# Kernel tuning notes

Hardware: AMD Instinct MI355X
Metric: run time of the kernel (lower is better)

The kernel has to match this reference:

```python
import jax, jax.numpy as jnp
import numpy as np

EPS = 1e-5
R_MAX = 2.0
KPTS = 4

def silu(x):
    return x * jax.nn.sigmoid(x)

def conv1x1(x, w):  # w: (O, I)
    return jnp.einsum('oi,bihw->bohw', w, x)

def dwconv3(x, k):  # k: (C, 1, 3, 3), depthwise
    return jax.lax.conv_general_dilated(x, k, (1, 1), 'SAME',
        feature_group_count=x.shape[1], dimension_numbers=('NCHW', 'OIHW', 'NCHW'))

def conv3x3(x, k):  # k: (O, I, 3, 3)
    return jax.lax.conv_general_dilated(x, k, (1, 1), 'SAME',
        dimension_numbers=('NCHW', 'OIHW', 'NCHW'))

def bn_eval(x, g, b, m, v):
    scale = g / jnp.sqrt(v + EPS)
    return x * scale[None, :, None, None] + (b - m * scale)[None, :, None, None]

def ds_block(x, dw, pw, g, b, m, v):  # _DS: dwconv3 -> 1x1 -> BN -> SiLU
    return silu(bn_eval(conv1x1(dwconv3(x, dw), pw), g, b, m, v))

def offset_attn_head(q, w1, w2, b2):
    h = silu(conv3x3(q, w1))
    out = conv1x1(h, w2) + b2[None, :, None, None]
    B, _, H, W = out.shape
    off = out[:, :2 * KPTS].reshape(B, KPTS, 2, H, W)
    w = jax.nn.softmax(out[:, 2 * KPTS:].reshape(B, KPTS, H, W), axis=1)
    return off, w

def make_base_grid(Hf, Wf, Hc, Wc):
    yy, xx = jnp.meshgrid(jnp.arange(Hf, dtype=jnp.float32),
                          jnp.arange(Wf, dtype=jnp.float32), indexing='ij')
    xc = (xx + 0.5) * (Wc / Wf) - 0.5
    yc = (yy + 0.5) * (Hc / Hf) - 0.5
    gx = 2.0 * xc / max(Wc - 1, 1) - 1.0
    gy = 2.0 * yc / max(Hc - 1, 1) - 1.0
    return jnp.stack((gx, gy), axis=-1)  # (Hf, Wf, 2)

def avgpool(x, f):  # exact adaptive_avg_pool2d when H,W divisible by f
    B, C, H, W = x.shape
    return x.reshape(B, C, H // f, f, W // f, f).mean(axis=(3, 5))

def _gather(imgf, idx):  # imgf (C, HW), idx (K, Hf, Wf) -> (C, K, Hf, Wf)
    return imgf[:, idx]

def deform_sample(coarse, off, w, base, r_max=R_MAX):
    # bilinear grid_sample, padding_mode='border', align_corners=True
    B, C, Hc, Wc = coarse.shape
    K = off.shape[1]
    step_x = 2.0 / max(Wc - 1, 1)
    step_y = 2.0 / max(Hc - 1, 1)
    gx = base[..., 0][None, None] + jnp.tanh(off[:, :, 0]) * (r_max * step_x)  # (B,K,Hf,Wf)
    gy = base[..., 1][None, None] + jnp.tanh(off[:, :, 1]) * (r_max * step_y)
    ix = jnp.clip((gx + 1.0) * 0.5 * (Wc - 1), 0.0, Wc - 1)  # border padding = clamp
    iy = jnp.clip((gy + 1.0) * 0.5 * (Hc - 1), 0.0, Hc - 1)
    x0 = jnp.floor(ix); y0 = jnp.floor(iy)
    wx = (ix - x0)[:, None]  # (B,1,K,Hf,Wf)
    wy = (iy - y0)[:, None]
    x0i = x0.astype(jnp.int32); y0i = y0.astype(jnp.int32)
    x1i = jnp.minimum(x0i + 1, Wc - 1); y1i = jnp.minimum(y0i + 1, Hc - 1)
    imgf = coarse.reshape(B, C, Hc * Wc)
    g = jax.vmap(_gather)
    v00 = g(imgf, y0i * Wc + x0i)  # (B,C,K,Hf,Wf)
    v01 = g(imgf, y0i * Wc + x1i)
    v10 = g(imgf, y1i * Wc + x0i)
    v11 = g(imgf, y1i * Wc + x1i)
    samp = (v00 * (1 - wx) * (1 - wy) + v01 * wx * (1 - wy)
            + v10 * (1 - wx) * wy + v11 * wx * wy)
    return jnp.einsum('bkhw,bckhw->bchw', w, samp)

def csdm(x, ds0_dw, ds0_pw, ds0_g, ds0_b, ds0_m, ds0_v,
         ds1_dw, ds1_pw, ds1_g, ds1_b, ds1_m, ds1_v,
         ds2_dw, ds2_pw, ds2_g, ds2_b, ds2_m, ds2_v,
         qproj_w, h1_w1, h1_w2, h1_b2, h2_w1, h2_w2, h2_b2,
         r_w1, r_b1, r_w2, r_b2, final_w):
    B, C, H, W = x.shape
    s1 = avgpool(x, 2)
    s2 = avgpool(x, 4)
    z0 = ds_block(x,  ds0_dw, ds0_pw, ds0_g, ds0_b, ds0_m, ds0_v)
    z1 = ds_block(s1, ds1_dw, ds1_pw, ds1_g, ds1_b, ds1_m, ds1_v)
    z2 = ds_block(s2, ds2_dw, ds2_pw, ds2_g, ds2_b, ds2_m, ds2_v)
    q = conv1x1(z0, qproj_w)
    off1, w1 = offset_attn_head(q, h1_w1, h1_w2, h1_b2)
    off2, w2 = offset_attn_head(q, h2_w1, h2_w2, h2_b2)
    base1 = make_base_grid(H, W, z1.shape[2], z1.shape[3])
    base2 = make_base_grid(H, W, z2.shape[2], z2.shape[3])
    y1 = deform_sample(z1, off1, w1, base1)
    y2 = deform_sample(z2, off2, w2, base2)
    d0 = z0.mean(axis=(2, 3))
    d1 = y1.mean(axis=(2, 3))
    d2 = y2.mean(axis=(2, 3))
    hid = silu(jnp.concatenate([d0, d1, d2], axis=-1) @ r_w1 + r_b1)
    alpha = jax.nn.softmax(hid @ r_w2 + r_b2, axis=-1)  # (B, 3)
    a = alpha[:, :, None, None, None]
    out = a[:, 0] * z0 + a[:, 1] * y1 + a[:, 2] * y2
    return x + conv1x1(out, final_w)

def setup_inputs() -> dict:
    key = jax.random.key(0)
    B, C, H, W = 4, 32, 256, 256
    h, hr = 16, 32  # head hidden = max(4, int(C*0.5)); router hidden = max(16, C)
    ks = jax.random.split(key, 40)
    n = lambda i, shape, s=0.2: jax.random.normal(ks[i], shape, jnp.float32) * s
    inp = {'x': jax.random.normal(ks[0], (B, C, H, W), jnp.float32)}
    for j, p in enumerate(['ds0', 'ds1', 'ds2']):
        b = 1 + 6 * j
        inp[p + '_dw'] = n(b, (C, 1, 3, 3))
        inp[p + '_pw'] = n(b + 1, (C, C))
        inp[p + '_g'] = jnp.ones((C,), jnp.float32)
        inp[p + '_b'] = jnp.zeros((C,), jnp.float32)
        inp[p + '_m'] = n(b + 4, (C,), 0.1)
        inp[p + '_v'] = 1.0 + jax.random.uniform(ks[b + 5], (C,), jnp.float32) * 0.1
    inp['qproj_w'] = n(20, (C, C))
    inp['h1_w1'] = n(21, (h, C, 3, 3)); inp['h1_w2'] = n(22, (3 * KPTS, h)); inp['h1_b2'] = n(23, (3 * KPTS,), 0.1)
    inp['h2_w1'] = n(24, (h, C, 3, 3)); inp['h2_w2'] = n(25, (3 * KPTS, h)); inp['h2_b2'] = n(26, (3 * KPTS,), 0.1)
    inp['r_w1'] = n(27, (3 * C, hr)); inp['r_b1'] = n(28, (hr,), 0.1)
    inp['r_w2'] = n(29, (hr, 3)); inp['r_b2'] = n(30, (3,), 0.1)
    inp['final_w'] = n(31, (C, C))
    return inp

def reference(x, ds0_dw, ds0_pw, ds0_g, ds0_b, ds0_m, ds0_v,
              ds1_dw, ds1_pw, ds1_g, ds1_b, ds1_m, ds1_v,
              ds2_dw, ds2_pw, ds2_g, ds2_b, ds2_m, ds2_v,
              qproj_w, h1_w1, h1_w2, h1_b2, h2_w1, h2_w2, h2_b2,
              r_w1, r_b1, r_w2, r_b2, final_w):
    return csdm(x, ds0_dw, ds0_pw, ds0_g, ds0_b, ds0_m, ds0_v,
                ds1_dw, ds1_pw, ds1_g, ds1_b, ds1_m, ds1_v,
                ds2_dw, ds2_pw, ds2_g, ds2_b, ds2_m, ds2_v,
                qproj_w, h1_w1, h1_w2, h1_b2, h2_w1, h2_w2, h2_b2,
                r_w1, r_b1, r_w2, r_b2, final_w)
```

## Files before the change

kernel.cpp:

```cpp
#include <hip/hip_runtime.h>
#include <math.h>


constexpr int B = 4, C = 32, H = 256, W = 256;
constexpr int HW = H * W;
constexpr int H1 = 128, W1 = 128, HW1 = H1 * W1;
constexpr int H2 = 64,  W2 = 64,  HW2 = H2 * W2;
constexpr int CH = 16;
constexpr int CO = 12;
constexpr int TILE = 16;
constexpr int HALO = 18;
constexpr int TAREA = HALO * HALO;
constexpr int WP = 258;

typedef unsigned short ushort_t;
typedef __attribute__((ext_vector_type(8))) short bf16x8;
typedef __attribute__((ext_vector_type(4))) float f32x4;
typedef __attribute__((ext_vector_type(2))) float v2f;

static __device__ __forceinline__ float fast_rcp(float x) { return __builtin_amdgcn_rcpf(x); }
static __device__ __forceinline__ float silu_f(float x) { return x * fast_rcp(1.0f + __expf(-x)); }
static __device__ __forceinline__ v2f silu2(v2f x) {
    v2f r; r.x = silu_f(x.x); r.y = silu_f(x.y); return r;
}
static __device__ __forceinline__ float tanh_f(float x) {
    float xc = fminf(fmaxf(x, -15.0f), 15.0f);
    float e = __expf(2.0f * xc);
    return (e - 1.0f) * fast_rcp(e + 1.0f);
}
static __device__ __forceinline__ ushort_t f2b(float f) {
    unsigned u = __float_as_uint(f);
    return (ushort_t)((u + 0x7fffu + ((u >> 16) & 1u)) >> 16);
}
static __device__ __forceinline__ float bl(unsigned u) { return __uint_as_float(u << 16); }
static __device__ __forceinline__ float bh(unsigned u) { return __uint_as_float(u & 0xffff0000u); }

static __device__ __forceinline__ float red8_ch(float v0, float v1, float v2, float v3,
                                                float v4, float v5, float v6, float v7,
                                                int lane) {
    bool q0 = (lane & 1) != 0, q1 = (lane & 2) != 0, q2 = (lane & 4) != 0;
    float a0 = (q0 ? v4 : v0) + __shfl_xor(q0 ? v0 : v4, 1, 64);
    float a1 = (q0 ? v5 : v1) + __shfl_xor(q0 ? v1 : v5, 1, 64);
    float a2 = (q0 ? v6 : v2) + __shfl_xor(q0 ? v2 : v6, 1, 64);
    float a3 = (q0 ? v7 : v3) + __shfl_xor(q0 ? v3 : v7, 1, 64);
    float c0 = (q1 ? a2 : a0) + __shfl_xor(q1 ? a0 : a2, 2, 64);
    float c1 = (q1 ? a3 : a1) + __shfl_xor(q1 ? a1 : a3, 2, 64);
    float e  = (q2 ? c1 : c0) + __shfl_xor(q2 ? c0 : c1, 4, 64);
    e += __shfl_xor(e, 8, 64);
    e += __shfl_xor(e, 16, 64);
    e += __shfl_xor(e, 32, 64);
    return e;
}

__global__ void pre_kernel(const float* __restrict__ x, float* __restrict__ s1,
                           float* __restrict__ s2,
                           ushort_t* __restrict__ qpad, float* __restrict__ dall,
                           const float* __restrict__ h1w1, const float* __restrict__ h2w1,
                           ushort_t* __restrict__ w1ra, ushort_t* __restrict__ w1rb) {
    int idx = blockIdx.x * blockDim.x + threadIdx.x;
    constexpr int NP = B * C * HW1;
    constexpr int NP2 = B * C * HW2;
    if (idx < NP) {
        int wo = idx % W1; int t = idx / W1;
        int ho = t % H1;   t /= H1;
        const float* src = x + ((size_t)t * H + (size_t)ho * 2) * W + (size_t)wo * 2;
        s1[idx] = (src[0] + src[1] + src[W] + src[W + 1]) * 0.25f;
        return;
    }
    int i = idx - NP;
    if (i < NP2) {
        int wo = i % W2; int t = i / W2;
        int ho = t % H2;   t /= H2;
        const float* src = x + ((size_t)t * H + (size_t)ho * 4) * W + (size_t)wo * 4;
        float s = 0.0f;
#pragma unroll
        for (int r = 0; r < 4; ++r) {
            const float* rp = src + (size_t)r * W;
            s += (rp[0] + rp[1]) + (rp[2] + rp[3]);
        }
        s2[i] = s * 0.0625f;
        return;
    }
    i -= NP2;
    if (i < 4112) {
        int b = i / 1028, r = i % 1028;
        int y, xx;
        if (r < 258)      { y = 0;           xx = r; }
        else if (r < 516) { y = 257;         xx = r - 258; }
        else if (r < 772) { y = r - 516 + 1; xx = 0; }
        else              { y = r - 772 + 1; xx = 257; }
        uint4 z4 = {0, 0, 0, 0};
        uint4* p = (uint4*)(qpad + (((size_t)b * WP + y) * WP + xx) * 32);
        p[0] = z4; p[1] = z4; p[2] = z4; p[3] = z4;
        return;
    }
    i -= 4112;
    if (i < 512) { dall[i] = 0.0f; return; }
    i -= 512;
    if (i < 4608) {
        int o = i / 288, k = i - o * 288;
        int j = k >> 5, ci = k & 31;
        w1ra[i] = f2b(h1w1[(o * C + ci) * 9 + j]);
        return;
    }
    i -= 4608;
    if (i < 4608) {
        int o = i / 288, k = i - o * 288;
        int j = k >> 5, ci = k & 31;
        w1rb[i] = f2b(h2w1[(o * C + ci) * 9 + j]);
    }
}

struct DsParams {
    const float* in; const float* dw; const float* pw;
    const float* g;  const float* b;  const float* m; const float* v;
};

__global__ __launch_bounds__(256, 4) void fused_ds_all_kernel(
        DsParams P0, DsParams P1, DsParams P2, const float* __restrict__ qw,
        float* __restrict__ z0out, ushort_t* __restrict__ z1cl,
        ushort_t* __restrict__ z2cl, ushort_t* __restrict__ qout,
        float* __restrict__ dall) {
    __shared__ unsigned tileu[16 * TAREA];
    __shared__ v2f dwp[16 * 9];
    __shared__ v2f pwp[C * 16];
    __shared__ v2f qwp[C * 16];
    __shared__ v2f scale2[16], shift2[16];
    __shared__ float zsum[4][32];

    int bx = blockIdx.x;
    int level = (bx < 1024) ? 0 : (bx < 1280 ? 1 : 2);
    int rel = bx - ((level == 0) ? 0 : (level == 1 ? 1024 : 1280));
    int Hs = (level == 0) ? H : (level == 1 ? H1 : H2);
    int Ws = Hs;
    int tilesX = Ws / TILE;
    int tilesT = tilesX * (Hs / TILE);
    int b = rel / tilesT;
    int tile = rel - b * tilesT;
    int ox = (tile % tilesX) * TILE;
    int oy = (tile / tilesX) * TILE;
    DsParams P = (level == 0) ? P0 : (level == 1 ? P1 : P2);
    int HWs = Hs * Ws;
    int tid = threadIdx.x;

    for (int i = tid; i < 16 * 9; i += 256) {
        int c2 = i / 9, j = i - c2 * 9;
        dwp[i] = (v2f){P.dw[(2 * c2) * 9 + j], P.dw[(2 * c2 + 1) * 9 + j]};
    }
    for (int i = tid; i < C * 16; i += 256) {
        int ci = i >> 4, o2 = i & 15;
        pwp[i] = (v2f){P.pw[(2 * o2) * C + ci], P.pw[(2 * o2 + 1) * C + ci]};
        if (level == 0) qwp[i] = (v2f){qw[(2 * o2) * C + ci], qw[(2 * o2 + 1) * C + ci]};
    }
    if (tid < 16) {
        float s0 = P.g[2 * tid] * rsqrtf(P.v[2 * tid] + 1e-5f);
        float s1v = P.g[2 * tid + 1] * rsqrtf(P.v[2 * tid + 1] + 1e-5f);
        scale2[tid] = (v2f){s0, s1v};
        shift2[tid] = (v2f){P.b[2 * tid] - P.m[2 * tid] * s0,
                            P.b[2 * tid + 1] - P.m[2 * tid + 1] * s1v};
    }
    const float* src = P.in + (size_t)b * C * HWs;
    for (int i = tid; i < 16 * TAREA; i += 256) {
        int c2 = i / TAREA, r = i - c2 * TAREA;
        int yy = r / HALO, xx = r - yy * HALO;
        int gy = oy - 1 + yy, gx = ox - 1 + xx;
        float v0 = 0.0f, v1 = 0.0f;
        if (gy >= 0 && gy < Hs && gx >= 0 && gx < Ws) {
            const float* sp = src + (size_t)(2 * c2) * HWs + gy * Ws + gx;
            v0 = sp[0]; v1 = sp[HWs];
        }
        tileu[i] = (unsigned)f2b(v0) | ((unsigned)f2b(v1) << 16);
    }
    __syncthreads();

    int tx = tid & 15, ty = tid >> 4;
    int off[9];
#pragma unroll
    for (int jy = 0; jy < 3; ++jy)
#pragma unroll
        for (int jx = 0; jx < 3; ++jx)
            off[jy * 3 + jx] = (ty + jy) * HALO + tx + jx;

    v2f t2[16];
#pragma unroll
    for (int c2 = 0; c2 < 16; ++c2) {
        v2f s = {0.0f, 0.0f};
        const unsigned* tp = tileu + c2 * TAREA;
#pragma unroll
        for (int j = 0; j < 9; ++j) {
            unsigned u = tp[off[j]];
            v2f val = {bl(u), bh(u)};
            s += dwp[c2 * 9 + j] * val;
        }
        t2[c2] = s;
    }

    v2f acc2[16];
#pragma unroll
    for (int o2 = 0; o2 < 16; ++o2) acc2[o2] = (v2f){0.0f, 0.0f};
#pragma unroll
    for (int i2 = 0; i2 < 16; ++i2) {
        float ta = t2[i2].x, tb = t2[i2].y;
        const v2f* r0 = pwp + (2 * i2) * 16;
        const v2f* r1 = r0 + 16;
#pragma unroll
        for (int o2 = 0; o2 < 16; ++o2)
            acc2[o2] += r0[o2] * ta + r1[o2] * tb;
    }
#pragma unroll
    for (int o2 = 0; o2 < 16; ++o2)
        acc2[o2] = silu2(acc2[o2] * scale2[o2] + shift2[o2]);

    int px = ox + tx, py = oy + ty;
    int p = py * Ws + px;
    if (level > 0) {
        ushort_t* outcl = (level == 1) ? z1cl : z2cl;
        unsigned up[16];
#pragma unroll
        for (int j = 0; j < 16; ++j)
            up[j] = (unsigned)f2b(acc2[j].x) | ((unsigned)f2b(acc2[j].y) << 16);
        uint4* dst = (uint4*)(outcl + ((size_t)b * HWs + p) * C);
#pragma unroll
        for (int j = 0; j < 4; ++j)
            dst[j] = make_uint4(up[4 * j], up[4 * j + 1], up[4 * j + 2], up[4 * j + 3]);
    } else {
        float* dst = z0out + (size_t)b * C * HWs + p;
#pragma unroll
        for (int o2 = 0; o2 < 16; ++o2) {
            dst[(size_t)(2 * o2) * HWs] = acc2[o2].x;
            dst[(size_t)(2 * o2 + 1) * HWs] = acc2[o2].y;
        }
        v2f q2[16];
#pragma unroll
        for (int o2 = 0; o2 < 16; ++o2) q2[o2] = (v2f){0.0f, 0.0f};
#pragma unroll
        for (int i2 = 0; i2 < 16; ++i2) {
            float ta = acc2[i2].x, tb = acc2[i2].y;
            const v2f* r0 = qwp + (2 * i2) * 16;
            const v2f* r1 = r0 + 16;
#pragma unroll
            for (int o2 = 0; o2 < 16; ++o2)
                q2[o2] += r0[o2] * ta + r1[o2] * tb;
        }
        unsigned up[16];
#pragma unroll
        for (int j = 0; j < 16; ++j)
            up[j] = (unsigned)f2b(q2[j].x) | ((unsigned)f2b(q2[j].y) << 16);
        uint4* qd = (uint4*)(qout + (((size_t)b * WP + py + 1) * WP + px + 1) * 32);
#pragma unroll
        for (int j = 0; j < 4; ++j)
            qd[j] = make_uint4(up[4 * j], up[4 * j + 1], up[4 * j + 2], up[4 * j + 3]);
        int lane = tid & 63, wv = tid >> 6;
#pragma unroll
        for (int gq = 0; gq < 4; ++gq) {
            float s = red8_ch(acc2[4 * gq].x,     acc2[4 * gq].y,
                              acc2[4 * gq + 1].x, acc2[4 * gq + 1].y,
                              acc2[4 * gq + 2].x, acc2[4 * gq + 2].y,
                              acc2[4 * gq + 3].x, acc2[4 * gq + 3].y, lane);
            if (lane < 8)
                zsum[wv][8 * gq + ((lane & 1) * 4 + (lane & 2) + ((lane >> 2) & 1))] = s;
        }
        __syncthreads();
        if (tid < 32)
            atomicAdd(&dall[b * 96 + tid],
                      (zsum[0][tid] + zsum[1][tid] + zsum[2][tid] + zsum[3][tid]) * (1.0f / HW));
    }
}

template<int HC, int WC>
static __device__ __forceinline__ void calc_off(const float* o12, int px, int py,
                                                int* zoff, float* wgt) {
    float mx = fmaxf(fmaxf(o12[8], o12[9]), fmaxf(o12[10], o12[11]));
    float e0 = __expf(o12[8] - mx), e1 = __expf(o12[9] - mx);
    float e2 = __expf(o12[10] - mx), e3 = __expf(o12[11] - mx);
    float inv = fast_rcp(e0 + e1 + e2 + e3);
    float wk4[4] = {e0 * inv, e1 * inv, e2 * inv, e3 * inv};
    float xc = (px + 0.5f) * ((float)WC / (float)W) - 0.5f;
    float yc = (py + 0.5f) * ((float)HC / (float)H) - 0.5f;
#pragma unroll
    for (int k = 0; k < 4; ++k) {
        float ix = fminf(fmaxf(xc + 2.0f * tanh_f(o12[2 * k]),     0.0f), (float)(WC - 1));
        float iy = fminf(fmaxf(yc + 2.0f * tanh_f(o12[2 * k + 1]), 0.0f), (float)(HC - 1));
        float x0f = floorf(ix), y0f = floorf(iy);
        int x0 = (int)x0f, y0 = (int)y0f;
        int x1 = min(x0 + 1, WC - 1), y1 = min(y0 + 1, HC - 1);
        float wx = ix - x0f, wy = iy - y0f;
        float wk = wk4[k];
        zoff[4 * k + 0] = (y0 * WC + x0) * C; wgt[4 * k + 0] = (1.0f - wx) * (1.0f - wy) * wk;
        zoff[4 * k + 1] = (y0 * WC + x1) * C; wgt[4 * k + 1] = wx * (1.0f - wy) * wk;
        zoff[4 * k + 2] = (y1 * WC + x0) * C; wgt[4 * k + 2] = (1.0f - wx) * wy * wk;
        zoff[4 * k + 3] = (y1 * WC + x1) * C; wgt[4 * k + 3] = wx * wy * wk;
    }
}

__global__ __launch_bounds__(256, 4) void head_deform_kernel(
        const ushort_t* __restrict__ qpad,
        const ushort_t* __restrict__ z1, const ushort_t* __restrict__ z2,
        const ushort_t* __restrict__ w1ra, const ushort_t* __restrict__ w1rb,
        const float* __restrict__ w2a, const float* __restrict__ b2a,
        const float* __restrict__ w2b, const float* __restrict__ b2b,
        float* __restrict__ y1, float* __restrict__ y2, float* __restrict__ dall) {
    __shared__ __align__(16) char smem[TAREA * C * 2];
    ushort_t* tile = (ushort_t*)smem;
    unsigned* hidw = (unsigned*)smem;
    float (*ysum)[32] = (float (*)[32])(smem + 9216);
    int tid = threadIdx.x, b = blockIdx.y, hsel = blockIdx.z;
    int ox = (blockIdx.x & 15) * TILE, oy = (blockIdx.x >> 4) * TILE;
    int lane = tid & 63, wv = tid >> 6;
    int n15 = lane & 15, quad = lane >> 4;
    int tx = tid & 15, ty = tid >> 4;

    {
        const ushort_t* base = qpad + ((size_t)b * WP + oy) * WP * 32;
        uint4* tl = (uint4*)tile;
        for (int i = tid; i < 1296; i += 256) {
            int yy = i / 72, r = i - yy * 72;
            tl[i] = *(const uint4*)(base + ((size_t)yy * WP + ox) * 32 + r * 8);
        }
    }
    __syncthreads();

    const ushort_t* w1r = hsel ? w1rb : w1ra;
    bf16x8 af[9];
#pragma unroll
    for (int j = 0; j < 9; ++j)
        af[j] = *(const bf16x8*)(w1r + n15 * 288 + j * 32 + quad * 8);
    unsigned pk[8];
#pragma unroll
    for (int g = 0; g < 4; ++g) {
        int yrow = wv * 4 + g;
        f32x4 acc = {0.0f, 0.0f, 0.0f, 0.0f};
#pragma unroll
        for (int jy = 0; jy < 3; ++jy)
#pragma unroll
            for (int jx = 0; jx < 3; ++jx) {
                const bf16x8* bp = (const bf16x8*)(tile +
                    ((yrow + jy) * HALO + n15 + jx) * 32 + quad * 8);
                acc = __builtin_amdgcn_mfma_f32_16x16x32_bf16(
                    af[jy * 3 + jx], *bp, acc, 0, 0, 0);
            }
        pk[2 * g]     = (unsigned)f2b(acc[0]) | ((unsigned)f2b(acc[1]) << 16);
        pk[2 * g + 1] = (unsigned)f2b(acc[2]) | ((unsigned)f2b(acc[3]) << 16);
    }
    __syncthreads();
#pragma unroll
    for (int g = 0; g < 4; ++g) {
        int pxl = (wv * 4 + g) * 16 + n15;
        hidw[pxl * 9 + quad * 2]     = pk[2 * g];
        hidw[pxl * 9 + quad * 2 + 1] = pk[2 * g + 1];
    }
    float hid[CH];
#pragma unroll
    for (int j = 0; j < 8; ++j) {
        unsigned u = hidw[tid * 9 + j];
        hid[2 * j]     = silu_f(bl(u));
        hid[2 * j + 1] = silu_f(bh(u));
    }

    const float* w2 = hsel ? w2b : w2a;
    const float* bs = hsel ? b2b : b2a;
    float o12[CO];
#pragma unroll
    for (int j = 0; j < CO; ++j) {
        float a = bs[j];
#pragma unroll
        for (int i = 0; i < CH; ++i) a += w2[j * CH + i] * hid[i];
        o12[j] = a;
    }
    int px = ox + tx, py = oy + ty;
    int off[16]; float wg[16];
    if (hsel == 0) calc_off<H1, W1>(o12, px, py, off, wg);
    else           calc_off<H2, W2>(o12, px, py, off, wg);

    const ushort_t* zb = hsel ? z2 + (size_t)b * HW2 * C : z1 + (size_t)b * HW1 * C;
    int p = py * W + px;
    float* d = (hsel ? y2 : y1) + (size_t)b * C * HW + p;

#pragma unroll
    for (int c8 = 0; c8 < 4; ++c8) {
        uint4 vv[16];
#pragma unroll
        for (int j = 0; j < 16; ++j)
            vv[j] = *(const uint4*)(zb + off[j] + c8 * 8);
        f32x4 lo = {0.0f, 0.0f, 0.0f, 0.0f};
        f32x4 hi = {0.0f, 0.0f, 0.0f, 0.0f};
#pragma unroll
        for (int j = 0; j < 16; ++j) {
            float wj = wg[j];
            lo[0] += wj * bl(vv[j].x); lo[1] += wj * bh(vv[j].x);
            lo[2] += wj * bl(vv[j].y); lo[3] += wj * bh(vv[j].y);
            hi[0] += wj * bl(vv[j].z); hi[1] += wj * bh(vv[j].z);
            hi[2] += wj * bl(vv[j].w); hi[3] += wj * bh(vv[j].w);
        }
#pragma unroll
        for (int k = 0; k < 4; ++k) {
            d[(size_t)(c8 * 8 + k) * HW]     = lo[k];
            d[(size_t)(c8 * 8 + 4 + k) * HW] = hi[k];
        }
        float s = red8_ch(lo[0], lo[1], lo[2], lo[3], hi[0], hi[1], hi[2], hi[3], lane);
        if (lane < 8)
            ysum[wv][c8 * 8 + ((lane & 1) * 4 + (lane & 2) + ((lane >> 2) & 1))] = s;
    }
    __syncthreads();
    if (tid < 32) {
        float s = ysum[0][tid] + ysum[1][tid] + ysum[2][tid] + ysum[3][tid];
        atomicAdd(&dall[b * 96 + 32 + hsel * 32 + tid], s * (1.0f / HW));
    }
}

__global__ void gate_kernel(const float* __restrict__ dall,
                            const float* __restrict__ w1, const float* __restrict__ b1,
                            const float* __restrict__ w2, const float* __restrict__ b2,
                            float* __restrict__ alpha) {
    __shared__ float hid[B][32];
    int tid = threadIdx.x;
    int b = tid >> 5, j = tid & 31;
    float a = b1[j];
    for (int k = 0; k < 96; ++k) a += dall[b * 96 + k] * w1[k * 32 + j];
    hid[b][j] = silu_f(a);
    __syncthreads();
    if (j == 0) {
        float lg[3];
#pragma unroll
        for (int t = 0; t < 3; ++t) {
            float acc = b2[t];
            for (int jj = 0; jj < 32; ++jj) acc += hid[b][jj] * w2[jj * 3 + t];
            lg[t] = acc;
        }
        float mx = fmaxf(lg[0], fmaxf(lg[1], lg[2]));
        float e0 = __expf(lg[0] - mx), e1 = __expf(lg[1] - mx), e2 = __expf(lg[2] - mx);
        float inv = fast_rcp(e0 + e1 + e2);
        alpha[b * 3 + 0] = e0 * inv;
        alpha[b * 3 + 1] = e1 * inv;
        alpha[b * 3 + 2] = e2 * inv;
    }
}

__global__ __launch_bounds__(256, 4) void final_kernel(
        const float* __restrict__ x,
        const float* __restrict__ z0, const float* __restrict__ y1,
        const float* __restrict__ y2, const float* __restrict__ alpha,
        const float* __restrict__ fw, float* __restrict__ out) {
    __shared__ float ws[C * C];
    for (int i = threadIdx.x; i < C * C; i += blockDim.x) ws[i] = fw[i];
    __syncthreads();
    int idx = blockIdx.x * blockDim.x + threadIdx.x;
    constexpr int HP = HW / 2;
    if (idx >= B * HP) return;
    int b = idx / HP, p = (idx - b * HP) * 2;
    float a0 = alpha[b * 3], a1 = alpha[b * 3 + 1], a2 = alpha[b * 3 + 2];
    size_t base = (size_t)b * C * HW + p;
    v2f mix[C];
#pragma unroll
    for (int i = 0; i < C; ++i) {
        size_t e = base + (size_t)i * HW;
        v2f za = *(const v2f*)(z0 + e);
        v2f ya = *(const v2f*)(y1 + e);
        v2f yb = *(const v2f*)(y2 + e);
        mix[i] = a0 * za + a1 * ya + a2 * yb;
    }
#pragma unroll 4
    for (int o = 0; o < C; ++o) {
        v2f acc = {0.0f, 0.0f};
#pragma unroll
        for (int i = 0; i < C; ++i) acc += ws[o * C + i] * mix[i];
        size_t e = base + (size_t)o * HW;
        v2f xr = *(const v2f*)(x + e);
        *(v2f*)(out + e) = acc + xr;
    }
}

extern "C" void kernel_launch(void* const* d_in, const int* in_sizes, int n_in,
                              void* d_out, int out_size, void* d_ws, size_t ws_size,
                              hipStream_t stream) {
    const float* x       = (const float*)d_in[0];
    const float* ds_dw[3] = {(const float*)d_in[1],  (const float*)d_in[7],  (const float*)d_in[13]};
    const float* ds_pw[3] = {(const float*)d_in[2],  (const float*)d_in[8],  (const float*)d_in[14]};
    const float* ds_g[3]  = {(const float*)d_in[3],  (const float*)d_in[9],  (const float*)d_in[15]};
    const float* ds_b[3]  = {(const float*)d_in[4],  (const float*)d_in[10], (const float*)d_in[16]};
    const float* ds_m[3]  = {(const float*)d_in[5],  (const float*)d_in[11], (const float*)d_in[17]};
    const float* ds_v[3]  = {(const float*)d_in[6],  (const float*)d_in[12], (const float*)d_in[18]};
    const float* qproj_w = (const float*)d_in[19];
    const float* h1_w1   = (const float*)d_in[20];
    const float* h1_w2   = (const float*)d_in[21];
    const float* h1_b2   = (const float*)d_in[22];
    const float* h2_w1   = (const float*)d_in[23];
    const float* h2_w2   = (const float*)d_in[24];
    const float* h2_b2   = (const float*)d_in[25];
    const float* r_w1    = (const float*)d_in[26];
    const float* r_b1    = (const float*)d_in[27];
    const float* r_w2    = (const float*)d_in[28];
    const float* r_b2    = (const float*)d_in[29];
    const float* final_w = (const float*)d_in[30];
    float* out = (float*)d_out;

    constexpr size_t N0 = (size_t)B * C * HW;
    constexpr size_t N1 = (size_t)B * C * HW1;
    constexpr size_t N2 = (size_t)B * C * HW2;
    constexpr size_t NQ = ((size_t)B * WP * WP * 32 + 1) / 2;

    float* w = (float*)d_ws;
    float* z0   = w; w += N0;
    float* y1   = w; w += N0;
    float* y2   = w; w += N0;
    ushort_t* z1cl = (ushort_t*)w; w += N1 / 2;
    ushort_t* z2cl = (ushort_t*)w; w += N2 / 2;
    float* s1   = w; w += N1;
    float* s2   = w; w += N2;
    ushort_t* qpad = (ushort_t*)w; w += NQ;
    ushort_t* w1ra = (ushort_t*)w; w += 2304;
    ushort_t* w1rb = (ushort_t*)w; w += 2304;
    float* dall  = w; w += 512;
    float* alpha = w; w += 16;
    (void)ws_size; (void)in_sizes; (void)n_in; (void)out_size;

    const int T = 256;
    auto g = [](size_t n, int t) { return (int)((n + t - 1) / t); };

    pre_kernel<<<g(N1 + N2 + 4112 + 512 + 9216, T), T, 0, stream>>>(
        x, s1, s2, qpad, dall, h1_w1, h2_w1, w1ra, w1rb);

    DsParams p0 = {x,  ds_dw[0], ds_pw[0], ds_g[0], ds_b[0], ds_m[0], ds_v[0]};
    DsParams p1 = {s1, ds_dw[1], ds_pw[1], ds_g[1], ds_b[1], ds_m[1], ds_v[1]};
    DsParams p2 = {s2, ds_dw[2], ds_pw[2], ds_g[2], ds_b[2], ds_m[2], ds_v[2]};
    fused_ds_all_kernel<<<1344, T, 0, stream>>>(
        p0, p1, p2, qproj_w, z0, z1cl, z2cl, qpad, dall);

    head_deform_kernel<<<dim3((H / TILE) * (W / TILE), B, 2), T, 0, stream>>>(
        qpad, z1cl, z2cl, w1ra, w1rb, h1_w2, h1_b2, h2_w2, h2_b2, y1, y2, dall);

    gate_kernel<<<1, 128, 0, stream>>>(dall, r_w1, r_b1, r_w2, r_b2, alpha);

    final_kernel<<<g((size_t)B * HW / 2, T), T, 0, stream>>>(x, z0, y1, y2, alpha, final_w, out);
}
```

Baseline: 299.2 us.

## Use bf16 MFMA for pointwise and qproj 1x1 convs in fused DS kernel

Moves the 32x32 pointwise convolution and the qproj projection in the fused depthwise-separable kernel from scalar FP32 FMAs to 16x16x32 bf16 MFMA instructions. Depthwise outputs are staged as bf16 in shared memory, which reuses the halo tile buffer, and pointwise weights are pre-converted to bf16 in pre_kernel. The aim is to cut ALU time and register pressure. In exchange it adds extra syncs, shared-memory round trips and bf16 rounding of intermediates, which may loosen accuracy.

```diff
diff --git a/kernel.cpp b/kernel.cpp
--- a/kernel.cpp
+++ b/kernel.cpp
@@ -20,9 +20,6 @@
 
 static __device__ __forceinline__ float fast_rcp(float x) { return __builtin_amdgcn_rcpf(x); }
 static __device__ __forceinline__ float silu_f(float x) { return x * fast_rcp(1.0f + __expf(-x)); }
-static __device__ __forceinline__ v2f silu2(v2f x) {
-    v2f r; r.x = silu_f(x.x); r.y = silu_f(x.y); return r;
-}
 static __device__ __forceinline__ float tanh_f(float x) {
     float xc = fminf(fmaxf(x, -15.0f), 15.0f);
     float e = __expf(2.0f * xc);
@@ -56,7 +53,10 @@
                            float* __restrict__ s2,
                            ushort_t* __restrict__ qpad, float* __restrict__ dall,
                            const float* __restrict__ h1w1, const float* __restrict__ h2w1,
-                           ushort_t* __restrict__ w1ra, ushort_t* __restrict__ w1rb) {
+                           ushort_t* __restrict__ w1ra, ushort_t* __restrict__ w1rb,
+                           const float* __restrict__ pw0, const float* __restrict__ pw1,
+                           const float* __restrict__ pw2, const float* __restrict__ qw,
+                           ushort_t* __restrict__ pwr) {
     int idx = blockIdx.x * blockDim.x + threadIdx.x;
     constexpr int NP = B * C * HW1;
     constexpr int NP2 = B * C * HW2;
@@ -108,24 +108,32 @@
         int o = i / 288, k = i - o * 288;
         int j = k >> 5, ci = k & 31;
         w1rb[i] = f2b(h2w1[(o * C + ci) * 9 + j]);
+        return;
+    }
+    i -= 4608;
+    if (i < 4096) {
+        int mm = i >> 10, k = i & 1023;
+        int o = k >> 5, ci = k & 31;
+        const float* wsrc = (mm == 0) ? pw0 : (mm == 1) ? pw1 : (mm == 2) ? pw2 : qw;
+        pwr[i] = f2b(wsrc[o * C + ci]);
     }
 }
 
 struct DsParams {
-    const float* in; const float* dw; const float* pw;
+    const float* in; const float* dw;
     const float* g;  const float* b;  const float* m; const float* v;
 };
 
 __global__ __launch_bounds__(256, 4) void fused_ds_all_kernel(
-        DsParams P0, DsParams P1, DsParams P2, const float* __restrict__ qw,
+        DsParams P0, DsParams P1, DsParams P2, const ushort_t* __restrict__ pwr,
         float* __restrict__ z0out, ushort_t* __restrict__ z1cl,
         ushort_t* __restrict__ z2cl, ushort_t* __restrict__ qout,
         float* __restrict__ dall) {
-    __shared__ unsigned tileu[16 * TAREA];
+    __shared__ __align__(16) char smem[16 * TAREA * 4];
+    unsigned* tileu = (unsigned*)smem;
+    ushort_t* bstg  = (ushort_t*)smem;
     __shared__ v2f dwp[16 * 9];
-    __shared__ v2f pwp[C * 16];
-    __shared__ v2f qwp[C * 16];
-    __shared__ v2f scale2[16], shift2[16];
+    __shared__ __align__(16) float sc[32], sh[32];
     __shared__ float zsum[4][32];
 
     int bx = blockIdx.x;
@@ -142,22 +150,18 @@
     DsParams P = (level == 0) ? P0 : (level == 1 ? P1 : P2);
     int HWs = Hs * Ws;
     int tid = threadIdx.x;
+    int lane = tid & 63, wv = tid >> 6;
+    int n15 = lane & 15, quad = lane >> 4;
+    int tx = tid & 15, ty = tid >> 4;
 
     for (int i = tid; i < 16 * 9; i += 256) {
         int c2 = i / 9, j = i - c2 * 9;
         dwp[i] = (v2f){P.dw[(2 * c2) * 9 + j], P.dw[(2 * c2 + 1) * 9 + j]};
     }
-    for (int i = tid; i < C * 16; i += 256) {
-        int ci = i >> 4, o2 = i & 15;
-        pwp[i] = (v2f){P.pw[(2 * o2) * C + ci], P.pw[(2 * o2 + 1) * C + ci]};
-        if (level == 0) qwp[i] = (v2f){qw[(2 * o2) * C + ci], qw[(2 * o2 + 1) * C + ci]};
-    }
-    if (tid < 16) {
-        float s0 = P.g[2 * tid] * rsqrtf(P.v[2 * tid] + 1e-5f);
-        float s1v = P.g[2 * tid + 1] * rsqrtf(P.v[2 * tid + 1] + 1e-5f);
-        scale2[tid] = (v2f){s0, s1v};
-        shift2[tid] = (v2f){P.b[2 * tid] - P.m[2 * tid] * s0,
-                            P.b[2 * tid + 1] - P.m[2 * tid + 1] * s1v};
+    if (tid < 32) {
+        float s0 = P.g[tid] * rsqrtf(P.v[tid] + 1e-5f);
+        sc[tid] = s0;
+        sh[tid] = P.b[tid] - P.m[tid] * s0;
     }
     const float* src = P.in + (size_t)b * C * HWs;
     for (int i = tid; i < 16 * TAREA; i += 256) {
@@ -173,7 +177,6 @@
     }
     __syncthreads();
 
-    int tx = tid & 15, ty = tid >> 4;
     int off[9];
 #pragma unroll
     for (int jy = 0; jy < 3; ++jy)
@@ -194,76 +197,124 @@
         }
         t2[c2] = s;
     }
-
-    v2f acc2[16];
-#pragma unroll
-    for (int o2 = 0; o2 < 16; ++o2) acc2[o2] = (v2f){0.0f, 0.0f};
-#pragma unroll
-    for (int i2 = 0; i2 < 16; ++i2) {
-        float ta = t2[i2].x, tb = t2[i2].y;
-        const v2f* r0 = pwp + (2 * i2) * 16;
-        const v2f* r1 = r0 + 16;
-#pragma unroll
-        for (int o2 = 0; o2 < 16; ++o2)
-            acc2[o2] += r0[o2] * ta + r1[o2] * tb;
-    }
-#pragma unroll
-    for (int o2 = 0; o2 < 16; ++o2)
-        acc2[o2] = silu2(acc2[o2] * scale2[o2] + shift2[o2]);
-
-    int px = ox + tx, py = oy + ty;
-    int p = py * Ws + px;
-    if (level > 0) {
-        ushort_t* outcl = (level == 1) ? z1cl : z2cl;
+    __syncthreads();
+
+    {
         unsigned up[16];
 #pragma unroll
         for (int j = 0; j < 16; ++j)
-            up[j] = (unsigned)f2b(acc2[j].x) | ((unsigned)f2b(acc2[j].y) << 16);
-        uint4* dst = (uint4*)(outcl + ((size_t)b * HWs + p) * C);
+            up[j] = (unsigned)f2b(t2[j].x) | ((unsigned)f2b(t2[j].y) << 16);
+        uint4* bw = (uint4*)(bstg + (size_t)tid * 40);
 #pragma unroll
         for (int j = 0; j < 4; ++j)
-            dst[j] = make_uint4(up[4 * j], up[4 * j + 1], up[4 * j + 2], up[4 * j + 3]);
-    } else {
-        float* dst = z0out + (size_t)b * C * HWs + p;
-#pragma unroll
-        for (int o2 = 0; o2 < 16; ++o2) {
-            dst[(size_t)(2 * o2) * HWs] = acc2[o2].x;
-            dst[(size_t)(2 * o2 + 1) * HWs] = acc2[o2].y;
-        }
-        v2f q2[16];
-#pragma unroll
-        for (int o2 = 0; o2 < 16; ++o2) q2[o2] = (v2f){0.0f, 0.0f};
-#pragma unroll
-        for (int i2 = 0; i2 < 16; ++i2) {
-            float ta = acc2[i2].x, tb = acc2[i2].y;
-            const v2f* r0 = qwp + (2 * i2) * 16;
-            const v2f* r1 = r0 + 16;
-#pragma unroll
-            for (int o2 = 0; o2 < 16; ++o2)
-                q2[o2] += r0[o2] * ta + r1[o2] * tb;
-        }
-        unsigned up[16];
-#pragma unroll
-        for (int j = 0; j < 16; ++j)
-            up[j] = (unsigned)f2b(q2[j].x) | ((unsigned)f2b(q2[j].y) << 16);
-        uint4* qd = (uint4*)(qout + (((size_t)b * WP + py + 1) * WP + px + 1) * 32);
-#pragma unroll
-        for (int j = 0; j < 4; ++j)
-            qd[j] = make_uint4(up[4 * j], up[4 * j + 1], up[4 * j + 2], up[4 * j + 3]);
-        int lane = tid & 63, wv = tid >> 6;
-#pragma unroll
-        for (int gq = 0; gq < 4; ++gq) {
-            float s = red8_ch(acc2[4 * gq].x,     acc2[4 * gq].y,
-                              acc2[4 * gq + 1].x, acc2[4 * gq + 1].y,
-                              acc2[4 * gq + 2].x, acc2[4 * gq + 2].y,
-                              acc2[4 * gq + 3].x, acc2[4 * gq + 3].y, lane);
-            if (lane < 8)
-                zsum[wv][8 * gq + ((lane & 1) * 4 + (lane & 2) + ((lane >> 2) & 1))] = s;
+            bw[j] = make_uint4(up[4 * j], up[4 * j + 1], up[4 * j + 2], up[4 * j + 3]);
+    }
+    __syncthreads();
+
+    const ushort_t* pwl = pwr + level * 1024;
+    bf16x8 apw0 = *(const bf16x8*)(pwl + n15 * 32 + quad * 8);
+    bf16x8 apw1 = *(const bf16x8*)(pwl + (16 + n15) * 32 + quad * 8);
+    f32x4 c1[4][2];
+#pragma unroll
+    for (int g4 = 0; g4 < 4; ++g4) {
+        bf16x8 bf = *(const bf16x8*)(bstg + ((wv * 4 + g4) * 16 + n15) * 40 + quad * 8);
+        f32x4 z = {0.0f, 0.0f, 0.0f, 0.0f};
+        c1[g4][0] = __builtin_amdgcn_mfma_f32_16x16x32_bf16(apw0, bf, z, 0, 0, 0);
+        c1[g4][1] = __builtin_amdgcn_mfma_f32_16x16x32_bf16(apw1, bf, z, 0, 0, 0);
+    }
+    f32x4 sc0 = *(const f32x4*)(sc + 4 * quad);
+    f32x4 sc1 = *(const f32x4*)(sc + 16 + 4 * quad);
+    f32x4 sh0 = *(const f32x4*)(sh + 4 * quad);
+    f32x4 sh1 = *(const f32x4*)(sh + 16 + 4 * quad);
+#pragma unroll
+    for (int g4 = 0; g4 < 4; ++g4)
+#pragma unroll
+        for (int r = 0; r < 4; ++r) {
+            c1[g4][0][r] = silu_f(c1[g4][0][r] * sc0[r] + sh0[r]);
+            c1[g4][1][r] = silu_f(c1[g4][1][r] * sc1[r] + sh1[r]);
+        }
+    __syncthreads();
+
+#pragma unroll
+    for (int g4 = 0; g4 < 4; ++g4) {
+        int px = (wv * 4 + g4) * 16 + n15;
+        unsigned* bp = (unsigned*)(bstg + px * 40 + 4 * quad);
+        bp[0] = (unsigned)f2b(c1[g4][0][0]) | ((unsigned)f2b(c1[g4][0][1]) << 16);
+        bp[1] = (unsigned)f2b(c1[g4][0][2]) | ((unsigned)f2b(c1[g4][0][3]) << 16);
+        unsigned* bp2 = (unsigned*)(bstg + px * 40 + 16 + 4 * quad);
+        bp2[0] = (unsigned)f2b(c1[g4][1][0]) | ((unsigned)f2b(c1[g4][1][1]) << 16);
+        bp2[1] = (unsigned)f2b(c1[g4][1][2]) | ((unsigned)f2b(c1[g4][1][3]) << 16);
+    }
+    __syncthreads();
+
+    if (level == 0) {
+        float* z0b = z0out + (size_t)b * C * HW;
+#pragma unroll
+        for (int g4 = 0; g4 < 4; ++g4) {
+            float* rp = z0b + (size_t)(oy + wv * 4 + g4) * W + ox + n15;
+#pragma unroll
+            for (int r = 0; r < 4; ++r) {
+                rp[(size_t)(4 * quad + r) * HW]      = c1[g4][0][r];
+                rp[(size_t)(16 + 4 * quad + r) * HW] = c1[g4][1][r];
+            }
+        }
+        float ms[8];
+#pragma unroll
+        for (int r = 0; r < 4; ++r) {
+            ms[r]     = (c1[0][0][r] + c1[1][0][r]) + (c1[2][0][r] + c1[3][0][r]);
+            ms[4 + r] = (c1[0][1][r] + c1[1][1][r]) + (c1[2][1][r] + c1[3][1][r]);
+        }
+#pragma unroll
+        for (int r = 0; r < 8; ++r) {
+            ms[r] += __shfl_xor(ms[r], 1, 64);
+            ms[r] += __shfl_xor(ms[r], 2, 64);
+            ms[r] += __shfl_xor(ms[r], 4, 64);
+            ms[r] += __shfl_xor(ms[r], 8, 64);
+        }
+        if (n15 == 0) {
+#pragma unroll
+            for (int r = 0; r < 4; ++r) {
+                zsum[wv][4 * quad + r]      = ms[r];
+                zsum[wv][16 + 4 * quad + r] = ms[4 + r];
+            }
+        }
+        const ushort_t* qwl = pwr + 3 * 1024;
+        bf16x8 aq0 = *(const bf16x8*)(qwl + n15 * 32 + quad * 8);
+        bf16x8 aq1 = *(const bf16x8*)(qwl + (16 + n15) * 32 + quad * 8);
+        f32x4 c2[4][2];
+#pragma unroll
+        for (int g4 = 0; g4 < 4; ++g4) {
+            bf16x8 bf = *(const bf16x8*)(bstg + ((wv * 4 + g4) * 16 + n15) * 40 + quad * 8);
+            f32x4 z = {0.0f, 0.0f, 0.0f, 0.0f};
+            c2[g4][0] = __builtin_amdgcn_mfma_f32_16x16x32_bf16(aq0, bf, z, 0, 0, 0);
+            c2[g4][1] = __builtin_amdgcn_mfma_f32_16x16x32_bf16(aq1, bf, z, 0, 0, 0);
         }
         __syncthreads();
+#pragma unroll
+        for (int g4 = 0; g4 < 4; ++g4) {
+            int px = (wv * 4 + g4) * 16 + n15;
+            unsigned* bp = (unsigned*)(bstg + px * 40 + 4 * quad);
+            bp[0] = (unsigned)f2b(c2[g4][0][0]) | ((unsigned)f2b(c2[g4][0][1]) << 16);
+            bp[1] = (unsigned)f2b(c2[g4][0][2]) | ((unsigned)f2b(c2[g4][0][3]) << 16);
+            unsigned* bp2 = (unsigned*)(bstg + px * 40 + 16 + 4 * quad);
+            bp2[0] = (unsigned)f2b(c2[g4][1][0]) | ((unsigned)f2b(c2[g4][1][1]) << 16);
+            bp2[1] = (unsigned)f2b(c2[g4][1][2]) | ((unsigned)f2b(c2[g4][1][3]) << 16);
+        }
+        __syncthreads();
+        const uint4* rb = (const uint4*)(bstg + (size_t)tid * 40);
+        uint4 q0 = rb[0], q1 = rb[1], q2 = rb[2], q3 = rb[3];
+        uint4* qd = (uint4*)(qout + (((size_t)b * WP + oy + ty + 1) * WP + ox + tx + 1) * 32);
+        qd[0] = q0; qd[1] = q1; qd[2] = q2; qd[3] = q3;
         if (tid < 32)
             atomicAdd(&dall[b * 96 + tid],
                       (zsum[0][tid] + zsum[1][tid] + zsum[2][tid] + zsum[3][tid]) * (1.0f / HW));
+    } else {
+        ushort_t* outcl = (level == 1) ? z1cl : z2cl;
+        const uint4* rb = (const uint4*)(bstg + (size_t)tid * 40);
+        uint4 q0 = rb[0], q1 = rb[1], q2 = rb[2], q3 = rb[3];
+        int p = (oy + ty) * Ws + ox + tx;
+        uint4* dst = (uint4*)(outcl + ((size_t)b * HWs + p) * C);
+        dst[0] = q0; dst[1] = q1; dst[2] = q2; dst[3] = q3;
     }
 }
 
@@ -510,6 +561,7 @@
     ushort_t* qpad = (ushort_t*)w; w += NQ;
     ushort_t* w1ra = (ushort_t*)w; w += 2304;
     ushort_t* w1rb = (ushort_t*)w; w += 2304;
+    ushort_t* pwr  = (ushort_t*)w; w += 2048;
     float* dall  = w; w += 512;
     float* alpha = w; w += 16;
     (void)ws_size; (void)in_sizes; (void)n_in; (void)out_size;
@@ -517,14 +569,15 @@
     const int T = 256;
     auto g = [](size_t n, int t) { return (int)((n + t - 1) / t); };
 
-    pre_kernel<<<g(N1 + N2 + 4112 + 512 + 9216, T), T, 0, stream>>>(
-        x, s1, s2, qpad, dall, h1_w1, h2_w1, w1ra, w1rb);
-
-    DsParams p0 = {x,  ds_dw[0], ds_pw[0], ds_g[0], ds_b[0], ds_m[0], ds_v[0]};
-    DsParams p1 = {s1, ds_dw[1], ds_pw[1], ds_g[1], ds_b[1], ds_m[1], ds_v[1]};
-    DsParams p2 = {s2, ds_dw[2], ds_pw[2], ds_g[2], ds_b[2], ds_m[2], ds_v[2]};
+    pre_kernel<<<g(N1 + N2 + 4112 + 512 + 9216 + 4096, T), T, 0, stream>>>(
+        x, s1, s2, qpad, dall, h1_w1, h2_w1, w1ra, w1rb,
+        ds_pw[0], ds_pw[1], ds_pw[2], qproj_w, pwr);
+
+    DsParams p0 = {x,  ds_dw[0], ds_g[0], ds_b[0], ds_m[0], ds_v[0]};
+    DsParams p1 = {s1, ds_dw[1], ds_g[1], ds_b[1], ds_m[1], ds_v[1]};
+    DsParams p2 = {s2, ds_dw[2], ds_g[2], ds_b[2], ds_m[2], ds_v[2]};
     fused_ds_all_kernel<<<1344, T, 0, stream>>>(
-        p0, p1, p2, qproj_w, z0, z1cl, z2cl, qpad, dall);
+        p0, p1, p2, pwr, z0, z1cl, z2cl, qpad, dall);
 
     head_deform_kernel<<<dim3((H / TILE) * (W / TILE), B, 2), T, 0, stream>>>(
         qpad, z1cl, z2cl, w1ra, w1rb, h1_w2, h1_b2, h2_w2, h2_b2, y1, y2, dall);
```

Measured after the change: 270.6 us. -9.5%, faster.
